# Kernel optimization log

Measured on AMD Instinct MI355X. Metric: run time of the kernel, lower is better.

Reference implementation:

```python
import jax, jax.numpy as jnp
import numpy as np
import math

EMBED = 512
NUM_CLASSES = 100000
BATCH = 512
SCALE = 64.0
MARGIN = 0.5
COS_M = math.cos(MARGIN)
SIN_M = math.sin(MARGIN)
THRESHOLD = math.cos(math.pi - MARGIN)
MARGIN_MULT = math.sin(math.pi - MARGIN) * MARGIN
EPS = 1e-12  # F.normalize eps


def setup_inputs() -> dict:
    key = jax.random.key(0)
    k1, k2, k3 = jax.random.split(key, 3)
    embeddings = jax.random.normal(k1, (BATCH, EMBED), dtype=jnp.float32)
    labels = jax.random.randint(k2, (BATCH,), 0, NUM_CLASSES, dtype=jnp.int64)
    # xavier-uniform-like init for weight (num_classes, embedding_size)
    limit = math.sqrt(6.0 / (NUM_CLASSES + EMBED))
    weight = jax.random.uniform(k3, (NUM_CLASSES, EMBED), dtype=jnp.float32,
                                minval=-limit, maxval=limit)
    return {"embeddings": embeddings, "labels": labels, "weight": weight}


def _l2_normalize(x, axis):
    norm = jnp.sqrt(jnp.sum(x * x, axis=axis, keepdims=True))
    return x / jnp.maximum(norm, EPS)


def reference(embeddings, labels, weight):
    e = _l2_normalize(embeddings, axis=1)          # (B, D)
    w = _l2_normalize(weight, axis=1)              # (C, D)
    cosine = jnp.einsum('bd,cd->bc', e, w)         # (B, C)
    sine = jnp.sqrt(jnp.clip(1.0 - cosine * cosine, 0.0, None))
    phi = cosine * COS_M - sine * SIN_M
    # easy_margin=False branch
    phi = jnp.where(cosine > THRESHOLD, phi, cosine - MARGIN_MULT)
    one_hot = jax.nn.one_hot(labels, NUM_CLASSES, dtype=cosine.dtype)
    logits = SCALE * (one_hot * phi + (1.0 - one_hot) * cosine)
    logp = jax.nn.log_softmax(logits, axis=1)      # (B, C)
    nll = -jnp.take_along_axis(logp, labels[:, None], axis=1)[:, 0]
    return jnp.mean(nll)
```

## Files before the change

kernel.cpp:

```cpp
#include <hip/hip_runtime.h>
#include <hip/hip_bf16.h>
#include <math.h>

#define BATCH 512
#define EMBED 512
#define NCLS  100000
#define NCG   128
#define NBLK  512

typedef __attribute__((ext_vector_type(4)))  float f32x4;
typedef __attribute__((ext_vector_type(16))) float f32x16;
typedef __attribute__((ext_vector_type(2)))  long  i64x2;

constexpr float kCOS_M = 0.8775825618903728f;
constexpr float kSIN_M = 0.4794255386042030f;
constexpr float kTHR   = -0.8775825618903728f;
constexpr float kMM    = 0.2397127693021015f;

#define BARRIER() asm volatile("s_waitcnt lgkmcnt(0)\n\ts_barrier" ::: "memory")

__global__ void knorm_e(const float* __restrict__ E, unsigned char* __restrict__ En8) {
  int r = blockIdx.x;
  int l = threadIdx.x;
  const f32x4* src = (const f32x4*)(E + r * EMBED);
  f32x4 a = src[2 * l], b = src[2 * l + 1];
  float ss = a.x*a.x + a.y*a.y + a.z*a.z + a.w*a.w
           + b.x*b.x + b.y*b.y + b.z*b.z + b.w*b.w;
#pragma unroll
  for (int d = 1; d < 64; d <<= 1) ss += __shfl_xor(ss, d);
  float s = 16.0f / fmaxf(sqrtf(ss), 1e-12f);
  int w0 = __builtin_amdgcn_cvt_pk_fp8_f32(a.x * s, a.y * s, 0, false);
  w0     = __builtin_amdgcn_cvt_pk_fp8_f32(a.z * s, a.w * s, w0, true);
  int w1 = __builtin_amdgcn_cvt_pk_fp8_f32(b.x * s, b.y * s, 0, false);
  w1     = __builtin_amdgcn_cvt_pk_fp8_f32(b.z * s, b.w * s, w1, true);
  int slotL = (l & 1) * 16 + (l >> 2);
  int half  = (l >> 1) & 1;
  uint2 pk; pk.x = (unsigned)w0; pk.y = (unsigned)w1;
  *(uint2*)(En8 + r * 512 + (((slotL ^ (r & 31)) << 4) | (half << 3))) = pk;
}

__global__ void klabel(const float* __restrict__ E, const float* __restrict__ W,
                       const int* __restrict__ labels,
                       float* __restrict__ lcos, float* __restrict__ lphi)
{
  int r = blockIdx.x * 8 + (threadIdx.x >> 6);
  int l = threadIdx.x & 63;
  int lbl = labels[r];
  const float* ep = E + (size_t)r * EMBED + l * 8;
  const float* wp = W + (size_t)lbl * EMBED + l * 8;
  f32x4 e0 = *(const f32x4*)ep, e1 = *(const f32x4*)(ep + 4);
  f32x4 w0 = *(const f32x4*)wp, w1 = *(const f32x4*)(wp + 4);
  float dot = e0.x*w0.x + e0.y*w0.y + e0.z*w0.z + e0.w*w0.w
            + e1.x*w1.x + e1.y*w1.y + e1.z*w1.z + e1.w*w1.w;
  float se = e0.x*e0.x + e0.y*e0.y + e0.z*e0.z + e0.w*e0.w
           + e1.x*e1.x + e1.y*e1.y + e1.z*e1.z + e1.w*e1.w;
  float sw = w0.x*w0.x + w0.y*w0.y + w0.z*w0.z + w0.w*w0.w
           + w1.x*w1.x + w1.y*w1.y + w1.z*w1.z + w1.w*w1.w;
#pragma unroll
  for (int d = 1; d < 64; d <<= 1) {
    dot += __shfl_xor(dot, d); se += __shfl_xor(se, d); sw += __shfl_xor(sw, d);
  }
  float cosv = dot / (fmaxf(sqrtf(se), 1e-12f) * fmaxf(sqrtf(sw), 1e-12f));
  float cc = fminf(fmaxf(cosv, -1.f), 1.f);
  float sine = sqrtf(fmaxf(1.f - cc * cc, 0.f));
  float phi = (cosv > kTHR) ? (cosv * kCOS_M - sine * kSIN_M) : (cosv - kMM);
  if (l == 0) { lcos[r] = 64.f * cosv; lphi[r] = 64.f * phi; }
}

__global__ __launch_bounds__(512, 4) void kmain(
    const unsigned char* __restrict__ En8, const float* __restrict__ W,
    float* __restrict__ psum)
{
  __shared__ unsigned char Asm[128 * 512];
  __shared__ unsigned char Bsm[2][4096];
  __shared__ float rowsum[64];
  __shared__ float smemS[2][128];

  int bid = blockIdx.x;
  int xcd = bid & 7;
  int panel = (bid >> 3) & 3;
  int grp = bid >> 5;
  int cg = xcd | (grp << 3);

  int tid = threadIdx.x;
  int w = tid >> 6, l = tid & 63;
  int wr = w >> 1, wc = w & 1;
  int cl = l & 31, hi = l >> 5;
  int bcls = tid >> 3, bseg = tid & 7;

  int nt = (cg < 27) ? 13 : 12;
  int nph = nt * 8;

#pragma unroll
  for (int i = 0; i < 8; ++i) {
    int base = i * 8192 + w * 1024;
    __builtin_amdgcn_global_load_lds(
        (const __attribute__((address_space(1))) void*)(En8 + panel * 65536 + base + l * 16),
        (__attribute__((address_space(3))) void*)(&Asm[base]), 16, 0, 0);
  }

  f32x4 Ra0, Ra1, Rb0, Rb1;
  float ssq = 0.f;
  const int bregion = (bseg & 1) * 2 + (bseg >> 2);
  const int bhalf = (bseg >> 1) & 1;

  auto loadB = [&](int q, f32x4& v0, f32x4& v1) {
    int T = q >> 3;
    int cls = (cg + (T << 7)) * 64 + bcls;
    if (cls >= NCLS) cls = NCLS - 1;
    const float* p = W + (size_t)cls * EMBED + (q & 7) * 64 + bseg * 8;
    v0 = *(const f32x4*)p;
    v1 = *(const f32x4*)(p + 4);
  };

  auto writeB = [&](int buf, f32x4 v0, f32x4 v1) {
    float x0 = v0.x*128.f, x1 = v0.y*128.f, x2 = v0.z*128.f, x3 = v0.w*128.f;
    float x4 = v1.x*128.f, x5 = v1.y*128.f, x6 = v1.z*128.f, x7 = v1.w*128.f;
    ssq += x0*x0 + x1*x1 + x2*x2 + x3*x3 + x4*x4 + x5*x5 + x6*x6 + x7*x7;
    int w0 = __builtin_amdgcn_cvt_pk_fp8_f32(x0, x1, 0, false);
    w0     = __builtin_amdgcn_cvt_pk_fp8_f32(x2, x3, w0, true);
    int w1 = __builtin_amdgcn_cvt_pk_fp8_f32(x4, x5, 0, false);
    w1     = __builtin_amdgcn_cvt_pk_fp8_f32(x6, x7, w1, true);
    uint2 pk; pk.x = (unsigned)w0; pk.y = (unsigned)w1;
    *(uint2*)(&Bsm[buf][bregion * 1024 + bcls * 16 + bhalf * 8]) = pk;
  };

  f32x16 acc, S;
#pragma unroll
  for (int e = 0; e < 16; ++e) { acc[e] = 0.f; S[e] = 0.f; }

  const unsigned char* Abase = &Asm[(wr * 32 + cl) * 512];
  const int arowx = cl;
  const unsigned char* Bcol0 = &Bsm[0][(hi * 2) * 1024 + (wc * 32 + cl) * 16];
  const unsigned char* Bcol1 = &Bsm[1][(hi * 2) * 1024 + (wc * 32 + cl) * 16];

  auto compute = [&](const unsigned char* bb, int pt) {
    int t0 = pt * 2;
    i64x2 a0 = *(const i64x2*)(Abase + ((((hi << 4) | t0)       ^ arowx) << 4));
    i64x2 a1 = *(const i64x2*)(Abase + ((((hi << 4) | (t0 + 1)) ^ arowx) << 4));
    i64x2 b0 = *(const i64x2*)(bb);
    i64x2 b1 = *(const i64x2*)(bb + 1024);
    acc = __builtin_amdgcn_mfma_f32_32x32x16_fp8_fp8(a0[0], b0[0], acc, 0, 0, 0);
    acc = __builtin_amdgcn_mfma_f32_32x32x16_fp8_fp8(a0[1], b0[1], acc, 0, 0, 0);
    acc = __builtin_amdgcn_mfma_f32_32x32x16_fp8_fp8(a1[0], b1[0], acc, 0, 0, 0);
    acc = __builtin_amdgcn_mfma_f32_32x32x16_fp8_fp8(a1[1], b1[1], acc, 0, 0, 0);
  };

  auto ssqred = [&]() {
    float sq = ssq;
    sq += __shfl_xor(sq, 1); sq += __shfl_xor(sq, 2); sq += __shfl_xor(sq, 4);
    if (bseg == 0) rowsum[bcls] = sq;
    ssq = 0.f;
  };

  auto epilogue = [&](int T) {
    float rs = fmaxf(rowsum[wc * 32 + cl], 1e-30f);
    float rn = 4.0f / sqrtf(rs);
    int colg = (cg + (T << 7)) * 64 + wc * 32 + cl;
    float vm = (colg < NCLS) ? 1.0f : 0.0f;
#pragma unroll
    for (int e = 0; e < 16; ++e) {
      float v = __expf(fmaf(acc[e], rn, -64.0f));
      S[e] = fmaf(v, vm, S[e]);
      acc[e] = 0.f;
    }
  };

  loadB(0, Ra0, Ra1); loadB(1, Rb0, Rb1);
  writeB(0, Ra0, Ra1); writeB(1, Rb0, Rb1);
  loadB(2, Ra0, Ra1); loadB(3, Rb0, Rb1);
  asm volatile("s_waitcnt vmcnt(0)" ::: "memory");
  BARRIER();

  for (int p = 0; p < nph; p += 2) {
    compute(Bcol0, p & 7);
    BARRIER();
    if (p + 2 < nph) writeB(0, Ra0, Ra1);
    if (p + 4 < nph) loadB(p + 4, Ra0, Ra1);
    int po = p + 1;
    compute(Bcol1, po & 7);
    if ((po & 7) == 7) epilogue(po >> 3);
    BARRIER();
    if (po + 2 < nph) writeB(1, Rb0, Rb1);
    if (po + 4 < nph) loadB(po + 4, Rb0, Rb1);
    if (((po + 2) & 7) == 7) ssqred();
  }

#pragma unroll
  for (int e = 0; e < 16; ++e) {
    float v = S[e];
    v += __shfl_xor(v, 1); v += __shfl_xor(v, 2); v += __shfl_xor(v, 4);
    v += __shfl_xor(v, 8); v += __shfl_xor(v, 16);
    S[e] = v;
  }
  __syncthreads();
  if (cl == 0) {
#pragma unroll
    for (int e = 0; e < 16; ++e) {
      int row = wr * 32 + (e & 3) + 8 * (e >> 2) + 4 * hi;
      smemS[wc][row] = S[e];
    }
  }
  __syncthreads();
  if (tid < 128) psum[bid * 128 + tid] = smemS[0][tid] + smemS[1][tid];
}

__global__ void kred1(const float* __restrict__ psum, float* __restrict__ pp2) {
  int g = blockIdx.x;
  int r = threadIdx.x;
  int panel = g >> 4, grp = g & 15;
  float s = 0.f;
#pragma unroll
  for (int x = 0; x < 8; ++x) {
    int bid = x | (panel << 3) | (grp << 5);
    s += psum[bid * 128 + r];
  }
  pp2[g * 128 + r] = s;
}

__global__ void kfinal(const float* __restrict__ pp2, const float* __restrict__ lcos,
                       const float* __restrict__ lphi, float* __restrict__ out)
{
  int tid = threadIdx.x;
  int panel = tid >> 7, rl = tid & 127;
  float S = 0.f;
#pragma unroll
  for (int grp = 0; grp < 16; ++grp)
    S += pp2[((panel << 4) | grp) * 128 + rl];
  float lc = lcos[tid], lp = lphi[tid];
  S = S - __expf(lc - 64.f) + __expf(lp - 64.f);
  float nll = 64.f + __logf(S) - lp;
#pragma unroll
  for (int d = 1; d < 64; d <<= 1) nll += __shfl_xor(nll, d);
  __shared__ float sm[8];
  if ((tid & 63) == 0) sm[tid >> 6] = nll;
  __syncthreads();
  if (tid == 0) {
    float t = 0.f;
    for (int k = 0; k < 8; ++k) t += sm[k];
    out[0] = t * (1.0f / 512.0f);
  }
}

extern "C" void kernel_launch(void* const* d_in, const int* in_sizes, int n_in,
                              void* d_out, int out_size, void* d_ws, size_t ws_size,
                              hipStream_t stream)
{
  const float* E      = (const float*)d_in[0];
  const int*   labels = (const int*)d_in[1];
  const float* W      = (const float*)d_in[2];
  float* out = (float*)d_out;

  char* ws = (char*)d_ws;
  unsigned char* En8 = (unsigned char*)ws;
  float* psum = (float*)(ws + 262144);
  float* pp2  = (float*)(ws + 524288);
  float* lcos = (float*)(ws + 557056);
  float* lphi = lcos + BATCH;

  knorm_e<<<BATCH, 64, 0, stream>>>(E, En8);
  klabel <<<64, 512, 0, stream>>>(E, W, labels, lcos, lphi);
  kmain  <<<NBLK, 512, 0, stream>>>(En8, W, psum);
  kred1  <<<64, 128, 0, stream>>>(psum, pp2);
  kfinal <<<1, 512, 0, stream>>>(pp2, lcos, lphi, out);
}
```

Before: 89.12 us.

## Feed W fragments directly from registers into MFMA, drop B LDS staging and barriers

```diff
diff --git a/kernel.cpp b/kernel.cpp
--- a/kernel.cpp
+++ b/kernel.cpp
@@ -5,8 +5,6 @@
 #define BATCH 512
 #define EMBED 512
 #define NCLS  100000
-#define NCG   128
-#define NBLK  512
 
 typedef __attribute__((ext_vector_type(4)))  float f32x4;
 typedef __attribute__((ext_vector_type(16))) float f32x16;
@@ -17,7 +15,11 @@
 constexpr float kTHR   = -0.8775825618903728f;
 constexpr float kMM    = 0.2397127693021015f;
 
-#define BARRIER() asm volatile("s_waitcnt lgkmcnt(0)\n\ts_barrier" ::: "memory")
+__device__ __forceinline__ unsigned cvt4(float a, float b, float c, float d) {
+  int v = __builtin_amdgcn_cvt_pk_fp8_f32(a, b, 0, false);
+  v = __builtin_amdgcn_cvt_pk_fp8_f32(c, d, v, true);
+  return (unsigned)v;
+}
 
 __global__ void knorm_e(const float* __restrict__ E, unsigned char* __restrict__ En8) {
   int r = blockIdx.x;
@@ -29,13 +31,11 @@
 #pragma unroll
   for (int d = 1; d < 64; d <<= 1) ss += __shfl_xor(ss, d);
   float s = 16.0f / fmaxf(sqrtf(ss), 1e-12f);
-  int w0 = __builtin_amdgcn_cvt_pk_fp8_f32(a.x * s, a.y * s, 0, false);
-  w0     = __builtin_amdgcn_cvt_pk_fp8_f32(a.z * s, a.w * s, w0, true);
-  int w1 = __builtin_amdgcn_cvt_pk_fp8_f32(b.x * s, b.y * s, 0, false);
-  w1     = __builtin_amdgcn_cvt_pk_fp8_f32(b.z * s, b.w * s, w1, true);
+  uint2 pk;
+  pk.x = cvt4(a.x * s, a.y * s, a.z * s, a.w * s);
+  pk.y = cvt4(b.x * s, b.y * s, b.z * s, b.w * s);
   int slotL = (l & 1) * 16 + (l >> 2);
   int half  = (l >> 1) & 1;
-  uint2 pk; pk.x = (unsigned)w0; pk.y = (unsigned)w1;
   *(uint2*)(En8 + r * 512 + (((slotL ^ (r & 31)) << 4) | (half << 3))) = pk;
 }
 
@@ -67,29 +67,21 @@
   if (l == 0) { lcos[r] = 64.f * cosv; lphi[r] = 64.f * phi; }
 }
 
-__global__ __launch_bounds__(512, 4) void kmain(
+__global__ __launch_bounds__(512, 1) void kmain(
     const unsigned char* __restrict__ En8, const float* __restrict__ W,
     float* __restrict__ psum)
 {
   __shared__ unsigned char Asm[128 * 512];
-  __shared__ unsigned char Bsm[2][4096];
-  __shared__ float rowsum[64];
-  __shared__ float smemS[2][128];
+  __shared__ float smemS[8][128];
 
   int bid = blockIdx.x;
-  int xcd = bid & 7;
+  int xcd  = bid & 7;
   int panel = (bid >> 3) & 3;
-  int grp = bid >> 5;
-  int cg = xcd | (grp << 3);
+  int slot = bid >> 5;
 
   int tid = threadIdx.x;
   int w = tid >> 6, l = tid & 63;
-  int wr = w >> 1, wc = w & 1;
   int cl = l & 31, hi = l >> 5;
-  int bcls = tid >> 3, bseg = tid & 7;
-
-  int nt = (cg < 27) ? 13 : 12;
-  int nph = nt * 8;
 
 #pragma unroll
   for (int i = 0; i < 8; ++i) {
@@ -99,122 +91,137 @@
         (__attribute__((address_space(3))) void*)(&Asm[base]), 16, 0, 0);
   }
 
-  f32x4 Ra0, Ra1, Rb0, Rb1;
+  const unsigned char* Ap0 = (const unsigned char*)Asm + (size_t)cl * 512;
+  const unsigned char* Ap1 = Ap0 + 32 * 512;
+  const unsigned char* Ap2 = Ap0 + 64 * 512;
+  const unsigned char* Ap3 = Ap0 + 96 * 512;
+
+  int cnt = ((3124 - xcd) >> 3) + 1;
+  int sloc0 = slot * 8 + w;
+  int njobs = (cnt - sloc0 + 63) >> 6;
+  int strip0 = xcd + 8 * sloc0;
+  const size_t JSTR = (size_t)512 * 32 * EMBED;
+  const float* wjob = W + (size_t)(strip0 * 32 + cl) * EMBED + hi * 8;
+
+  f32x4 Ra0, Ra1, Ra2, Ra3, Rb0, Rb1, Rb2, Rb3;
+  f32x4 Rc0, Rc1, Rc2, Rc3, Rd0, Rd1, Rd2, Rd3;
+  f32x16 acc0, acc1, acc2, acc3, S0, S1, S2, S3;
+#pragma unroll
+  for (int e = 0; e < 16; ++e) {
+    acc0[e] = 0.f; acc1[e] = 0.f; acc2[e] = 0.f; acc3[e] = 0.f;
+    S0[e] = 0.f; S1[e] = 0.f; S2[e] = 0.f; S3[e] = 0.f;
+  }
   float ssq = 0.f;
-  const int bregion = (bseg & 1) * 2 + (bseg >> 2);
-  const int bhalf = (bseg >> 1) & 1;
-
-  auto loadB = [&](int q, f32x4& v0, f32x4& v1) {
-    int T = q >> 3;
-    int cls = (cg + (T << 7)) * 64 + bcls;
-    if (cls >= NCLS) cls = NCLS - 1;
-    const float* p = W + (size_t)cls * EMBED + (q & 7) * 64 + bseg * 8;
-    v0 = *(const f32x4*)p;
-    v1 = *(const f32x4*)(p + 4);
-  };
-
-  auto writeB = [&](int buf, f32x4 v0, f32x4 v1) {
-    float x0 = v0.x*128.f, x1 = v0.y*128.f, x2 = v0.z*128.f, x3 = v0.w*128.f;
-    float x4 = v1.x*128.f, x5 = v1.y*128.f, x6 = v1.z*128.f, x7 = v1.w*128.f;
-    ssq += x0*x0 + x1*x1 + x2*x2 + x3*x3 + x4*x4 + x5*x5 + x6*x6 + x7*x7;
-    int w0 = __builtin_amdgcn_cvt_pk_fp8_f32(x0, x1, 0, false);
-    w0     = __builtin_amdgcn_cvt_pk_fp8_f32(x2, x3, w0, true);
-    int w1 = __builtin_amdgcn_cvt_pk_fp8_f32(x4, x5, 0, false);
-    w1     = __builtin_amdgcn_cvt_pk_fp8_f32(x6, x7, w1, true);
-    uint2 pk; pk.x = (unsigned)w0; pk.y = (unsigned)w1;
-    *(uint2*)(&Bsm[buf][bregion * 1024 + bcls * 16 + bhalf * 8]) = pk;
-  };
-
-  f32x16 acc, S;
-#pragma unroll
-  for (int e = 0; e < 16; ++e) { acc[e] = 0.f; S[e] = 0.f; }
-
-  const unsigned char* Abase = &Asm[(wr * 32 + cl) * 512];
-  const int arowx = cl;
-  const unsigned char* Bcol0 = &Bsm[0][(hi * 2) * 1024 + (wc * 32 + cl) * 16];
-  const unsigned char* Bcol1 = &Bsm[1][(hi * 2) * 1024 + (wc * 32 + cl) * 16];
-
-  auto compute = [&](const unsigned char* bb, int pt) {
-    int t0 = pt * 2;
-    i64x2 a0 = *(const i64x2*)(Abase + ((((hi << 4) | t0)       ^ arowx) << 4));
-    i64x2 a1 = *(const i64x2*)(Abase + ((((hi << 4) | (t0 + 1)) ^ arowx) << 4));
-    i64x2 b0 = *(const i64x2*)(bb);
-    i64x2 b1 = *(const i64x2*)(bb + 1024);
-    acc = __builtin_amdgcn_mfma_f32_32x32x16_fp8_fp8(a0[0], b0[0], acc, 0, 0, 0);
-    acc = __builtin_amdgcn_mfma_f32_32x32x16_fp8_fp8(a0[1], b0[1], acc, 0, 0, 0);
-    acc = __builtin_amdgcn_mfma_f32_32x32x16_fp8_fp8(a1[0], b1[0], acc, 0, 0, 0);
-    acc = __builtin_amdgcn_mfma_f32_32x32x16_fp8_fp8(a1[1], b1[1], acc, 0, 0, 0);
-  };
-
-  auto ssqred = [&]() {
-    float sq = ssq;
-    sq += __shfl_xor(sq, 1); sq += __shfl_xor(sq, 2); sq += __shfl_xor(sq, 4);
-    if (bseg == 0) rowsum[bcls] = sq;
+
+#define LOADP(R0, R1, R2, R3, base, p)                    \
+  R0 = *(const f32x4*)((base) + (p) * 32);                \
+  R1 = *(const f32x4*)((base) + (p) * 32 + 4);            \
+  R2 = *(const f32x4*)((base) + (p) * 32 + 16);           \
+  R3 = *(const f32x4*)((base) + (p) * 32 + 20);
+
+#define COMPUTEP(R0, R1, R2, R3, p) {                                          \
+    ssq += R0.x*R0.x + R0.y*R0.y + R0.z*R0.z + R0.w*R0.w                       \
+         + R1.x*R1.x + R1.y*R1.y + R1.z*R1.z + R1.w*R1.w                       \
+         + R2.x*R2.x + R2.y*R2.y + R2.z*R2.z + R2.w*R2.w                       \
+         + R3.x*R3.x + R3.y*R3.y + R3.z*R3.z + R3.w*R3.w;                      \
+    uint2 bu0, bu1;                                                            \
+    bu0.x = cvt4(R0.x*128.f, R0.y*128.f, R0.z*128.f, R0.w*128.f);              \
+    bu0.y = cvt4(R1.x*128.f, R1.y*128.f, R1.z*128.f, R1.w*128.f);              \
+    bu1.x = cvt4(R2.x*128.f, R2.y*128.f, R2.z*128.f, R2.w*128.f);              \
+    bu1.y = cvt4(R3.x*128.f, R3.y*128.f, R3.z*128.f, R3.w*128.f);              \
+    long bop0 = __builtin_bit_cast(long, bu0);                                 \
+    long bop1 = __builtin_bit_cast(long, bu1);                                 \
+    const int so = ((((hi) << 4) | (p)) ^ cl) << 4;                            \
+    i64x2 a0 = *(const i64x2*)(Ap0 + so);                                      \
+    i64x2 a1 = *(const i64x2*)(Ap1 + so);                                      \
+    i64x2 a2 = *(const i64x2*)(Ap2 + so);                                      \
+    i64x2 a3 = *(const i64x2*)(Ap3 + so);                                      \
+    acc0 = __builtin_amdgcn_mfma_f32_32x32x16_fp8_fp8(a0[0], bop0, acc0,0,0,0);\
+    acc0 = __builtin_amdgcn_mfma_f32_32x32x16_fp8_fp8(a0[1], bop1, acc0,0,0,0);\
+    acc1 = __builtin_amdgcn_mfma_f32_32x32x16_fp8_fp8(a1[0], bop0, acc1,0,0,0);\
+    acc1 = __builtin_amdgcn_mfma_f32_32x32x16_fp8_fp8(a1[1], bop1, acc1,0,0,0);\
+    acc2 = __builtin_amdgcn_mfma_f32_32x32x16_fp8_fp8(a2[0], bop0, acc2,0,0,0);\
+    acc2 = __builtin_amdgcn_mfma_f32_32x32x16_fp8_fp8(a2[1], bop1, acc2,0,0,0);\
+    acc3 = __builtin_amdgcn_mfma_f32_32x32x16_fp8_fp8(a3[0], bop0, acc3,0,0,0);\
+    acc3 = __builtin_amdgcn_mfma_f32_32x32x16_fp8_fp8(a3[1], bop1, acc3,0,0,0);\
+  }
+
+  LOADP(Ra0, Ra1, Ra2, Ra3, wjob, 0)
+  LOADP(Rb0, Rb1, Rb2, Rb3, wjob, 1)
+  LOADP(Rc0, Rc1, Rc2, Rc3, wjob, 2)
+  LOADP(Rd0, Rd1, Rd2, Rd3, wjob, 3)
+  __syncthreads();
+
+  for (int j = 0; j < njobs; ++j) {
+    const float* wnx = (j + 1 < njobs) ? (wjob + JSTR) : W;
+    COMPUTEP(Ra0, Ra1, Ra2, Ra3, 0)  LOADP(Ra0, Ra1, Ra2, Ra3, wjob, 4)
+    COMPUTEP(Rb0, Rb1, Rb2, Rb3, 1)  LOADP(Rb0, Rb1, Rb2, Rb3, wjob, 5)
+    COMPUTEP(Rc0, Rc1, Rc2, Rc3, 2)  LOADP(Rc0, Rc1, Rc2, Rc3, wjob, 6)
+    COMPUTEP(Rd0, Rd1, Rd2, Rd3, 3)  LOADP(Rd0, Rd1, Rd2, Rd3, wjob, 7)
+    COMPUTEP(Ra0, Ra1, Ra2, Ra3, 4)  LOADP(Ra0, Ra1, Ra2, Ra3, wjob, 8)
+    COMPUTEP(Rb0, Rb1, Rb2, Rb3, 5)  LOADP(Rb0, Rb1, Rb2, Rb3, wjob, 9)
+    COMPUTEP(Rc0, Rc1, Rc2, Rc3, 6)  LOADP(Rc0, Rc1, Rc2, Rc3, wjob, 10)
+    COMPUTEP(Rd0, Rd1, Rd2, Rd3, 7)  LOADP(Rd0, Rd1, Rd2, Rd3, wjob, 11)
+    COMPUTEP(Ra0, Ra1, Ra2, Ra3, 8)  LOADP(Ra0, Ra1, Ra2, Ra3, wjob, 12)
+    COMPUTEP(Rb0, Rb1, Rb2, Rb3, 9)  LOADP(Rb0, Rb1, Rb2, Rb3, wjob, 13)
+    COMPUTEP(Rc0, Rc1, Rc2, Rc3, 10) LOADP(Rc0, Rc1, Rc2, Rc3, wjob, 14)
+    COMPUTEP(Rd0, Rd1, Rd2, Rd3, 11) LOADP(Rd0, Rd1, Rd2, Rd3, wjob, 15)
+    COMPUTEP(Ra0, Ra1, Ra2, Ra3, 12) LOADP(Ra0, Ra1, Ra2, Ra3, wnx, 0)
+    COMPUTEP(Rb0, Rb1, Rb2, Rb3, 13) LOADP(Rb0, Rb1, Rb2, Rb3, wnx, 1)
+    COMPUTEP(Rc0, Rc1, Rc2, Rc3, 14) LOADP(Rc0, Rc1, Rc2, Rc3, wnx, 2)
+    COMPUTEP(Rd0, Rd1, Rd2, Rd3, 15) LOADP(Rd0, Rd1, Rd2, Rd3, wnx, 3)
+    float rs = ssq + __shfl_xor(ssq, 32);
+    float rn = 0.03125f * rsqrtf(fmaxf(rs, 1e-30f));
+#pragma unroll
+    for (int e = 0; e < 16; ++e) {
+      S0[e] += __expf(fmaf(acc0[e], rn, -64.f)); acc0[e] = 0.f;
+      S1[e] += __expf(fmaf(acc1[e], rn, -64.f)); acc1[e] = 0.f;
+      S2[e] += __expf(fmaf(acc2[e], rn, -64.f)); acc2[e] = 0.f;
+      S3[e] += __expf(fmaf(acc3[e], rn, -64.f)); acc3[e] = 0.f;
+    }
     ssq = 0.f;
-  };
-
-  auto epilogue = [&](int T) {
-    float rs = fmaxf(rowsum[wc * 32 + cl], 1e-30f);
-    float rn = 4.0f / sqrtf(rs);
-    int colg = (cg + (T << 7)) * 64 + wc * 32 + cl;
-    float vm = (colg < NCLS) ? 1.0f : 0.0f;
+    wjob = wnx;
+  }
+#undef LOADP
+#undef COMPUTEP
+
+#pragma unroll
+  for (int e = 0; e < 16; ++e) {
+    float v0 = S0[e], v1 = S1[e], v2 = S2[e], v3 = S3[e];
+#pragma unroll
+    for (int d = 1; d < 32; d <<= 1) {
+      v0 += __shfl_xor(v0, d); v1 += __shfl_xor(v1, d);
+      v2 += __shfl_xor(v2, d); v3 += __shfl_xor(v3, d);
+    }
+    S0[e] = v0; S1[e] = v1; S2[e] = v2; S3[e] = v3;
+  }
+  if (cl == 0) {
 #pragma unroll
     for (int e = 0; e < 16; ++e) {
-      float v = __expf(fmaf(acc[e], rn, -64.0f));
-      S[e] = fmaf(v, vm, S[e]);
-      acc[e] = 0.f;
+      int rmap = (e & 3) + 8 * (e >> 2) + 4 * hi;
+      smemS[w][rmap]      = S0[e];
+      smemS[w][32 + rmap] = S1[e];
+      smemS[w][64 + rmap] = S2[e];
+      smemS[w][96 + rmap] = S3[e];
     }
-  };
-
-  loadB(0, Ra0, Ra1); loadB(1, Rb0, Rb1);
-  writeB(0, Ra0, Ra1); writeB(1, Rb0, Rb1);
-  loadB(2, Ra0, Ra1); loadB(3, Rb0, Rb1);
-  asm volatile("s_waitcnt vmcnt(0)" ::: "memory");
-  BARRIER();
-
-  for (int p = 0; p < nph; p += 2) {
-    compute(Bcol0, p & 7);
-    BARRIER();
-    if (p + 2 < nph) writeB(0, Ra0, Ra1);
-    if (p + 4 < nph) loadB(p + 4, Ra0, Ra1);
-    int po = p + 1;
-    compute(Bcol1, po & 7);
-    if ((po & 7) == 7) epilogue(po >> 3);
-    BARRIER();
-    if (po + 2 < nph) writeB(1, Rb0, Rb1);
-    if (po + 4 < nph) loadB(po + 4, Rb0, Rb1);
-    if (((po + 2) & 7) == 7) ssqred();
-  }
-
-#pragma unroll
-  for (int e = 0; e < 16; ++e) {
-    float v = S[e];
-    v += __shfl_xor(v, 1); v += __shfl_xor(v, 2); v += __shfl_xor(v, 4);
-    v += __shfl_xor(v, 8); v += __shfl_xor(v, 16);
-    S[e] = v;
   }
   __syncthreads();
-  if (cl == 0) {
-#pragma unroll
-    for (int e = 0; e < 16; ++e) {
-      int row = wr * 32 + (e & 3) + 8 * (e >> 2) + 4 * hi;
-      smemS[wc][row] = S[e];
-    }
-  }
-  __syncthreads();
-  if (tid < 128) psum[bid * 128 + tid] = smemS[0][tid] + smemS[1][tid];
+  if (tid < 128) {
+    float t = 0.f;
+#pragma unroll
+    for (int q = 0; q < 8; ++q) t += smemS[q][tid];
+    psum[bid * 128 + tid] = t;
+  }
 }
 
 __global__ void kred1(const float* __restrict__ psum, float* __restrict__ pp2) {
   int g = blockIdx.x;
   int r = threadIdx.x;
-  int panel = g >> 4, grp = g & 15;
+  int panel = g >> 3, xcd = g & 7;
   float s = 0.f;
 #pragma unroll
-  for (int x = 0; x < 8; ++x) {
-    int bid = x | (panel << 3) | (grp << 5);
-    s += psum[bid * 128 + r];
-  }
+  for (int slot = 0; slot < 8; ++slot)
+    s += psum[(xcd + 8 * panel + 32 * slot) * 128 + r];
   pp2[g * 128 + r] = s;
 }
 
@@ -225,8 +232,8 @@
   int panel = tid >> 7, rl = tid & 127;
   float S = 0.f;
 #pragma unroll
-  for (int grp = 0; grp < 16; ++grp)
-    S += pp2[((panel << 4) | grp) * 128 + rl];
+  for (int x = 0; x < 8; ++x)
+    S += pp2[(panel * 8 + x) * 128 + rl];
   float lc = lcos[tid], lp = lphi[tid];
   S = S - __expf(lc - 64.f) + __expf(lp - 64.f);
   float nll = 64.f + __logf(S) - lp;
@@ -254,13 +261,13 @@
   char* ws = (char*)d_ws;
   unsigned char* En8 = (unsigned char*)ws;
   float* psum = (float*)(ws + 262144);
-  float* pp2  = (float*)(ws + 524288);
-  float* lcos = (float*)(ws + 557056);
+  float* pp2  = (float*)(ws + 262144 + 131072);
+  float* lcos = (float*)(ws + 262144 + 131072 + 16384);
   float* lphi = lcos + BATCH;
 
   knorm_e<<<BATCH, 64, 0, stream>>>(E, En8);
   klabel <<<64, 512, 0, stream>>>(E, W, labels, lcos, lphi);
-  kmain  <<<NBLK, 512, 0, stream>>>(En8, W, psum);
-  kred1  <<<64, 128, 0, stream>>>(psum, pp2);
+  kmain  <<<256, 512, 0, stream>>>(En8, W, psum);
+  kred1  <<<32, 128, 0, stream>>>(psum, pp2);
   kfinal <<<1, 512, 0, stream>>>(pp2, lcos, lphi, out);
 }
```

Result: slower. 279.1 us (+213.2%).

## Hold normalized embedding panel in registers instead of LDS, unroll phase loop

Applied to the files above, without the earlier changes.

```diff
diff --git a/kernel.cpp b/kernel.cpp
--- a/kernel.cpp
+++ b/kernel.cpp
@@ -18,6 +18,12 @@
 constexpr float kMM    = 0.2397127693021015f;
 
 #define BARRIER() asm volatile("s_waitcnt lgkmcnt(0)\n\ts_barrier" ::: "memory")
+
+__device__ __forceinline__ unsigned cvt4(float a, float b, float c, float d) {
+  int v = __builtin_amdgcn_cvt_pk_fp8_f32(a, b, 0, false);
+  v = __builtin_amdgcn_cvt_pk_fp8_f32(c, d, v, true);
+  return (unsigned)v;
+}
 
 __global__ void knorm_e(const float* __restrict__ E, unsigned char* __restrict__ En8) {
   int r = blockIdx.x;
@@ -29,14 +35,12 @@
 #pragma unroll
   for (int d = 1; d < 64; d <<= 1) ss += __shfl_xor(ss, d);
   float s = 16.0f / fmaxf(sqrtf(ss), 1e-12f);
-  int w0 = __builtin_amdgcn_cvt_pk_fp8_f32(a.x * s, a.y * s, 0, false);
-  w0     = __builtin_amdgcn_cvt_pk_fp8_f32(a.z * s, a.w * s, w0, true);
-  int w1 = __builtin_amdgcn_cvt_pk_fp8_f32(b.x * s, b.y * s, 0, false);
-  w1     = __builtin_amdgcn_cvt_pk_fp8_f32(b.z * s, b.w * s, w1, true);
+  uint2 pk;
+  pk.x = cvt4(a.x * s, a.y * s, a.z * s, a.w * s);
+  pk.y = cvt4(b.x * s, b.y * s, b.z * s, b.w * s);
   int slotL = (l & 1) * 16 + (l >> 2);
   int half  = (l >> 1) & 1;
-  uint2 pk; pk.x = (unsigned)w0; pk.y = (unsigned)w1;
-  *(uint2*)(En8 + r * 512 + (((slotL ^ (r & 31)) << 4) | (half << 3))) = pk;
+  *(uint2*)(En8 + r * 512 + ((slotL << 4) | (half << 3))) = pk;
 }
 
 __global__ void klabel(const float* __restrict__ E, const float* __restrict__ W,
@@ -71,7 +75,6 @@
     const unsigned char* __restrict__ En8, const float* __restrict__ W,
     float* __restrict__ psum)
 {
-  __shared__ unsigned char Asm[128 * 512];
   __shared__ unsigned char Bsm[2][4096];
   __shared__ float rowsum[64];
   __shared__ float smemS[2][128];
@@ -89,102 +92,91 @@
   int bcls = tid >> 3, bseg = tid & 7;
 
   int nt = (cg < 27) ? 13 : 12;
-  int nph = nt * 8;
-
-#pragma unroll
-  for (int i = 0; i < 8; ++i) {
-    int base = i * 8192 + w * 1024;
-    __builtin_amdgcn_global_load_lds(
-        (const __attribute__((address_space(1))) void*)(En8 + panel * 65536 + base + l * 16),
-        (__attribute__((address_space(3))) void*)(&Asm[base]), 16, 0, 0);
-  }
+
+  int arow = panel * 128 + wr * 32 + cl;
+  const unsigned char* abase = En8 + arow * 512 + hi * 256;
+  i64x2 af[16];
+#pragma unroll
+  for (int t = 0; t < 16; ++t) af[t] = *(const i64x2*)(abase + t * 16);
+
+  float ssq = 0.f;
+  const int boff = ((bseg & 1) * 2 + (bseg >> 2)) * 1024 + bcls * 16 + ((bseg >> 1) & 1) * 8;
 
   f32x4 Ra0, Ra1, Rb0, Rb1;
-  float ssq = 0.f;
-  const int bregion = (bseg & 1) * 2 + (bseg >> 2);
-  const int bhalf = (bseg >> 1) & 1;
-
-  auto loadB = [&](int q, f32x4& v0, f32x4& v1) {
-    int T = q >> 3;
+  auto loadB = [&](int T, int kt, f32x4& v0, f32x4& v1) {
     int cls = (cg + (T << 7)) * 64 + bcls;
     if (cls >= NCLS) cls = NCLS - 1;
-    const float* p = W + (size_t)cls * EMBED + (q & 7) * 64 + bseg * 8;
+    const float* p = W + (size_t)cls * EMBED + kt * 64 + bseg * 8;
     v0 = *(const f32x4*)p;
     v1 = *(const f32x4*)(p + 4);
   };
-
   auto writeB = [&](int buf, f32x4 v0, f32x4 v1) {
     float x0 = v0.x*128.f, x1 = v0.y*128.f, x2 = v0.z*128.f, x3 = v0.w*128.f;
     float x4 = v1.x*128.f, x5 = v1.y*128.f, x6 = v1.z*128.f, x7 = v1.w*128.f;
     ssq += x0*x0 + x1*x1 + x2*x2 + x3*x3 + x4*x4 + x5*x5 + x6*x6 + x7*x7;
-    int w0 = __builtin_amdgcn_cvt_pk_fp8_f32(x0, x1, 0, false);
-    w0     = __builtin_amdgcn_cvt_pk_fp8_f32(x2, x3, w0, true);
-    int w1 = __builtin_amdgcn_cvt_pk_fp8_f32(x4, x5, 0, false);
-    w1     = __builtin_amdgcn_cvt_pk_fp8_f32(x6, x7, w1, true);
-    uint2 pk; pk.x = (unsigned)w0; pk.y = (unsigned)w1;
-    *(uint2*)(&Bsm[buf][bregion * 1024 + bcls * 16 + bhalf * 8]) = pk;
+    uint2 pk;
+    pk.x = cvt4(x0, x1, x2, x3);
+    pk.y = cvt4(x4, x5, x6, x7);
+    *(uint2*)(&Bsm[buf][boff]) = pk;
   };
 
   f32x16 acc, S;
 #pragma unroll
   for (int e = 0; e < 16; ++e) { acc[e] = 0.f; S[e] = 0.f; }
 
-  const unsigned char* Abase = &Asm[(wr * 32 + cl) * 512];
-  const int arowx = cl;
   const unsigned char* Bcol0 = &Bsm[0][(hi * 2) * 1024 + (wc * 32 + cl) * 16];
   const unsigned char* Bcol1 = &Bsm[1][(hi * 2) * 1024 + (wc * 32 + cl) * 16];
 
-  auto compute = [&](const unsigned char* bb, int pt) {
-    int t0 = pt * 2;
-    i64x2 a0 = *(const i64x2*)(Abase + ((((hi << 4) | t0)       ^ arowx) << 4));
-    i64x2 a1 = *(const i64x2*)(Abase + ((((hi << 4) | (t0 + 1)) ^ arowx) << 4));
-    i64x2 b0 = *(const i64x2*)(bb);
-    i64x2 b1 = *(const i64x2*)(bb + 1024);
-    acc = __builtin_amdgcn_mfma_f32_32x32x16_fp8_fp8(a0[0], b0[0], acc, 0, 0, 0);
-    acc = __builtin_amdgcn_mfma_f32_32x32x16_fp8_fp8(a0[1], b0[1], acc, 0, 0, 0);
-    acc = __builtin_amdgcn_mfma_f32_32x32x16_fp8_fp8(a1[0], b1[0], acc, 0, 0, 0);
-    acc = __builtin_amdgcn_mfma_f32_32x32x16_fp8_fp8(a1[1], b1[1], acc, 0, 0, 0);
-  };
-
-  auto ssqred = [&]() {
-    float sq = ssq;
-    sq += __shfl_xor(sq, 1); sq += __shfl_xor(sq, 2); sq += __shfl_xor(sq, 4);
-    if (bseg == 0) rowsum[bcls] = sq;
-    ssq = 0.f;
-  };
-
-  auto epilogue = [&](int T) {
-    float rs = fmaxf(rowsum[wc * 32 + cl], 1e-30f);
-    float rn = 4.0f / sqrtf(rs);
-    int colg = (cg + (T << 7)) * 64 + wc * 32 + cl;
-    float vm = (colg < NCLS) ? 1.0f : 0.0f;
-#pragma unroll
-    for (int e = 0; e < 16; ++e) {
-      float v = __expf(fmaf(acc[e], rn, -64.0f));
-      S[e] = fmaf(v, vm, S[e]);
-      acc[e] = 0.f;
-    }
-  };
-
-  loadB(0, Ra0, Ra1); loadB(1, Rb0, Rb1);
-  writeB(0, Ra0, Ra1); writeB(1, Rb0, Rb1);
-  loadB(2, Ra0, Ra1); loadB(3, Rb0, Rb1);
-  asm volatile("s_waitcnt vmcnt(0)" ::: "memory");
-  BARRIER();
-
-  for (int p = 0; p < nph; p += 2) {
-    compute(Bcol0, p & 7);
-    BARRIER();
-    if (p + 2 < nph) writeB(0, Ra0, Ra1);
-    if (p + 4 < nph) loadB(p + 4, Ra0, Ra1);
-    int po = p + 1;
-    compute(Bcol1, po & 7);
-    if ((po & 7) == 7) epilogue(po >> 3);
-    BARRIER();
-    if (po + 2 < nph) writeB(1, Rb0, Rb1);
-    if (po + 4 < nph) loadB(po + 4, Rb0, Rb1);
-    if (((po + 2) & 7) == 7) ssqred();
-  }
+  loadB(0, 0, Ra0, Ra1);
+  loadB(0, 1, Rb0, Rb1);
+  writeB(0, Ra0, Ra1);
+  writeB(1, Rb0, Rb1);
+  loadB(0, 2, Ra0, Ra1);
+  loadB(0, 3, Rb0, Rb1);
+  __syncthreads();
+
+#define PHASE(q, RS0, RS1) {                                                          \
+    const unsigned char* bb = ((q) & 1) ? Bcol1 : Bcol0;                              \
+    i64x2 b0 = *(const i64x2*)(bb);                                                   \
+    i64x2 b1 = *(const i64x2*)(bb + 1024);                                            \
+    acc = __builtin_amdgcn_mfma_f32_32x32x16_fp8_fp8(af[2*(q)][0],   b0[0], acc,0,0,0);\
+    acc = __builtin_amdgcn_mfma_f32_32x32x16_fp8_fp8(af[2*(q)][1],   b0[1], acc,0,0,0);\
+    acc = __builtin_amdgcn_mfma_f32_32x32x16_fp8_fp8(af[2*(q)+1][0], b1[0], acc,0,0,0);\
+    acc = __builtin_amdgcn_mfma_f32_32x32x16_fp8_fp8(af[2*(q)+1][1], b1[1], acc,0,0,0);\
+    if ((q) == 7) {                                                                    \
+      float rs = fmaxf(rowsum[wc * 32 + cl], 1e-30f);                                  \
+      float rn = 4.0f / sqrtf(rs);                                                     \
+      int colg = (cg + (T << 7)) * 64 + wc * 32 + cl;                                  \
+      float vm = (colg < NCLS) ? 1.0f : 0.0f;                                          \
+      _Pragma("unroll")                                                                \
+      for (int e = 0; e < 16; ++e) {                                                   \
+        S[e] = fmaf(__expf(fmaf(acc[e], rn, -64.0f)), vm, S[e]);                       \
+        acc[e] = 0.f;                                                                  \
+      }                                                                                \
+    }                                                                                  \
+    BARRIER();                                                                         \
+    if (!lastT || (q) < 6) writeB((q) & 1, RS0, RS1);                                  \
+    if (!lastT || (q) < 4) loadB(T + (((q) + 4) >> 3), ((q) + 4) & 7, RS0, RS1);       \
+    if ((q) == 5) {                                                                    \
+      float sq = ssq;                                                                  \
+      sq += __shfl_xor(sq, 1); sq += __shfl_xor(sq, 2); sq += __shfl_xor(sq, 4);       \
+      if (bseg == 0) rowsum[bcls] = sq;                                                \
+      ssq = 0.f;                                                                       \
+    }                                                                                  \
+  }
+
+  for (int T = 0; T < nt; ++T) {
+    bool lastT = (T == nt - 1);
+    PHASE(0, Ra0, Ra1)
+    PHASE(1, Rb0, Rb1)
+    PHASE(2, Ra0, Ra1)
+    PHASE(3, Rb0, Rb1)
+    PHASE(4, Ra0, Ra1)
+    PHASE(5, Rb0, Rb1)
+    PHASE(6, Ra0, Ra1)
+    PHASE(7, Rb0, Rb1)
+  }
+#undef PHASE
 
 #pragma unroll
   for (int e = 0; e < 16; ++e) {
```

Result: slower. 107.6 us (+20.7%).

## Enlarge main kernel tile to 256 rows with 1024-thread blocks

Applied to the files above, without the earlier changes.

```diff
diff --git a/kernel.cpp b/kernel.cpp
--- a/kernel.cpp
+++ b/kernel.cpp
@@ -6,7 +6,7 @@
 #define EMBED 512
 #define NCLS  100000
 #define NCG   128
-#define NBLK  512
+#define NBLK  256
 
 typedef __attribute__((ext_vector_type(4)))  float f32x4;
 typedef __attribute__((ext_vector_type(16))) float f32x16;
@@ -18,6 +18,12 @@
 constexpr float kMM    = 0.2397127693021015f;
 
 #define BARRIER() asm volatile("s_waitcnt lgkmcnt(0)\n\ts_barrier" ::: "memory")
+
+__device__ __forceinline__ unsigned cvt4(float a, float b, float c, float d) {
+  int v = __builtin_amdgcn_cvt_pk_fp8_f32(a, b, 0, false);
+  v = __builtin_amdgcn_cvt_pk_fp8_f32(c, d, v, true);
+  return (unsigned)v;
+}
 
 __global__ void knorm_e(const float* __restrict__ E, unsigned char* __restrict__ En8) {
   int r = blockIdx.x;
@@ -29,13 +35,11 @@
 #pragma unroll
   for (int d = 1; d < 64; d <<= 1) ss += __shfl_xor(ss, d);
   float s = 16.0f / fmaxf(sqrtf(ss), 1e-12f);
-  int w0 = __builtin_amdgcn_cvt_pk_fp8_f32(a.x * s, a.y * s, 0, false);
-  w0     = __builtin_amdgcn_cvt_pk_fp8_f32(a.z * s, a.w * s, w0, true);
-  int w1 = __builtin_amdgcn_cvt_pk_fp8_f32(b.x * s, b.y * s, 0, false);
-  w1     = __builtin_amdgcn_cvt_pk_fp8_f32(b.z * s, b.w * s, w1, true);
+  uint2 pk;
+  pk.x = cvt4(a.x * s, a.y * s, a.z * s, a.w * s);
+  pk.y = cvt4(b.x * s, b.y * s, b.z * s, b.w * s);
   int slotL = (l & 1) * 16 + (l >> 2);
   int half  = (l >> 1) & 1;
-  uint2 pk; pk.x = (unsigned)w0; pk.y = (unsigned)w1;
   *(uint2*)(En8 + r * 512 + (((slotL ^ (r & 31)) << 4) | (half << 3))) = pk;
 }
 
@@ -67,62 +71,52 @@
   if (l == 0) { lcos[r] = 64.f * cosv; lphi[r] = 64.f * phi; }
 }
 
-__global__ __launch_bounds__(512, 4) void kmain(
+__global__ __launch_bounds__(1024, 4) void kmain(
     const unsigned char* __restrict__ En8, const float* __restrict__ W,
     float* __restrict__ psum)
 {
-  __shared__ unsigned char Asm[128 * 512];
-  __shared__ unsigned char Bsm[2][4096];
+  __shared__ __align__(16) unsigned char Asm[256 * 512];
+  __shared__ __align__(16) unsigned char Bsm[2][4096];
   __shared__ float rowsum[64];
-  __shared__ float smemS[2][128];
+  __shared__ float smemS[2][256];
 
   int bid = blockIdx.x;
   int xcd = bid & 7;
-  int panel = (bid >> 3) & 3;
-  int grp = bid >> 5;
+  int panel = (bid >> 3) & 1;
+  int grp = bid >> 4;
   int cg = xcd | (grp << 3);
 
   int tid = threadIdx.x;
   int w = tid >> 6, l = tid & 63;
   int wr = w >> 1, wc = w & 1;
   int cl = l & 31, hi = l >> 5;
-  int bcls = tid >> 3, bseg = tid & 7;
+  int bcls = tid >> 4, bs = tid & 15;
 
   int nt = (cg < 27) ? 13 : 12;
   int nph = nt * 8;
 
 #pragma unroll
   for (int i = 0; i < 8; ++i) {
-    int base = i * 8192 + w * 1024;
+    int base = i * 16384 + w * 1024;
     __builtin_amdgcn_global_load_lds(
-        (const __attribute__((address_space(1))) void*)(En8 + panel * 65536 + base + l * 16),
+        (const __attribute__((address_space(1))) void*)(En8 + panel * 131072 + base + l * 16),
         (__attribute__((address_space(3))) void*)(&Asm[base]), 16, 0, 0);
   }
 
-  f32x4 Ra0, Ra1, Rb0, Rb1;
   float ssq = 0.f;
-  const int bregion = (bseg & 1) * 2 + (bseg >> 2);
-  const int bhalf = (bseg >> 1) & 1;
-
-  auto loadB = [&](int q, f32x4& v0, f32x4& v1) {
-    int T = q >> 3;
-    int cls = (cg + (T << 7)) * 64 + bcls;
+  const int boff = (((bs >> 1) & 1) * 2 + (bs >> 3)) * 1024 + bcls * 16
+                 + ((bs >> 2) & 1) * 8 + (bs & 1) * 4;
+
+  f32x4 Ra, Rb;
+  auto loadB = [&](int q, f32x4& v) {
+    int cls = (cg + ((q >> 3) << 7)) * 64 + bcls;
     if (cls >= NCLS) cls = NCLS - 1;
-    const float* p = W + (size_t)cls * EMBED + (q & 7) * 64 + bseg * 8;
-    v0 = *(const f32x4*)p;
-    v1 = *(const f32x4*)(p + 4);
-  };
-
-  auto writeB = [&](int buf, f32x4 v0, f32x4 v1) {
-    float x0 = v0.x*128.f, x1 = v0.y*128.f, x2 = v0.z*128.f, x3 = v0.w*128.f;
-    float x4 = v1.x*128.f, x5 = v1.y*128.f, x6 = v1.z*128.f, x7 = v1.w*128.f;
-    ssq += x0*x0 + x1*x1 + x2*x2 + x3*x3 + x4*x4 + x5*x5 + x6*x6 + x7*x7;
-    int w0 = __builtin_amdgcn_cvt_pk_fp8_f32(x0, x1, 0, false);
-    w0     = __builtin_amdgcn_cvt_pk_fp8_f32(x2, x3, w0, true);
-    int w1 = __builtin_amdgcn_cvt_pk_fp8_f32(x4, x5, 0, false);
-    w1     = __builtin_amdgcn_cvt_pk_fp8_f32(x6, x7, w1, true);
-    uint2 pk; pk.x = (unsigned)w0; pk.y = (unsigned)w1;
-    *(uint2*)(&Bsm[buf][bregion * 1024 + bcls * 16 + bhalf * 8]) = pk;
+    v = *(const f32x4*)(W + (size_t)cls * EMBED + (q & 7) * 64 + bs * 4);
+  };
+  auto writeB = [&](int buf, f32x4 v) {
+    float x0 = v.x*128.f, x1 = v.y*128.f, x2 = v.z*128.f, x3 = v.w*128.f;
+    ssq += x0*x0 + x1*x1 + x2*x2 + x3*x3;
+    *(unsigned*)(&Bsm[buf][boff]) = cvt4(x0, x1, x2, x3);
   };
 
   f32x16 acc, S;
@@ -130,14 +124,13 @@
   for (int e = 0; e < 16; ++e) { acc[e] = 0.f; S[e] = 0.f; }
 
   const unsigned char* Abase = &Asm[(wr * 32 + cl) * 512];
-  const int arowx = cl;
   const unsigned char* Bcol0 = &Bsm[0][(hi * 2) * 1024 + (wc * 32 + cl) * 16];
   const unsigned char* Bcol1 = &Bsm[1][(hi * 2) * 1024 + (wc * 32 + cl) * 16];
 
   auto compute = [&](const unsigned char* bb, int pt) {
     int t0 = pt * 2;
-    i64x2 a0 = *(const i64x2*)(Abase + ((((hi << 4) | t0)       ^ arowx) << 4));
-    i64x2 a1 = *(const i64x2*)(Abase + ((((hi << 4) | (t0 + 1)) ^ arowx) << 4));
+    i64x2 a0 = *(const i64x2*)(Abase + ((((hi << 4) | t0)       ^ cl) << 4));
+    i64x2 a1 = *(const i64x2*)(Abase + ((((hi << 4) | (t0 + 1)) ^ cl) << 4));
     i64x2 b0 = *(const i64x2*)(bb);
     i64x2 b1 = *(const i64x2*)(bb + 1024);
     acc = __builtin_amdgcn_mfma_f32_32x32x16_fp8_fp8(a0[0], b0[0], acc, 0, 0, 0);
@@ -148,8 +141,9 @@
 
   auto ssqred = [&]() {
     float sq = ssq;
-    sq += __shfl_xor(sq, 1); sq += __shfl_xor(sq, 2); sq += __shfl_xor(sq, 4);
-    if (bseg == 0) rowsum[bcls] = sq;
+    sq += __shfl_xor(sq, 1); sq += __shfl_xor(sq, 2);
+    sq += __shfl_xor(sq, 4); sq += __shfl_xor(sq, 8);
+    if (bs == 0) rowsum[bcls] = sq;
     ssq = 0.f;
   };
 
@@ -160,29 +154,28 @@
     float vm = (colg < NCLS) ? 1.0f : 0.0f;
 #pragma unroll
     for (int e = 0; e < 16; ++e) {
-      float v = __expf(fmaf(acc[e], rn, -64.0f));
-      S[e] = fmaf(v, vm, S[e]);
+      S[e] = fmaf(__expf(fmaf(acc[e], rn, -64.0f)), vm, S[e]);
       acc[e] = 0.f;
     }
   };
 
-  loadB(0, Ra0, Ra1); loadB(1, Rb0, Rb1);
-  writeB(0, Ra0, Ra1); writeB(1, Rb0, Rb1);
-  loadB(2, Ra0, Ra1); loadB(3, Rb0, Rb1);
+  loadB(0, Ra); loadB(1, Rb);
+  writeB(0, Ra); writeB(1, Rb);
+  loadB(2, Ra); loadB(3, Rb);
   asm volatile("s_waitcnt vmcnt(0)" ::: "memory");
   BARRIER();
 
   for (int p = 0; p < nph; p += 2) {
     compute(Bcol0, p & 7);
     BARRIER();
-    if (p + 2 < nph) writeB(0, Ra0, Ra1);
-    if (p + 4 < nph) loadB(p + 4, Ra0, Ra1);
+    if (p + 2 < nph) writeB(0, Ra);
+    if (p + 4 < nph) loadB(p + 4, Ra);
     int po = p + 1;
     compute(Bcol1, po & 7);
     if ((po & 7) == 7) epilogue(po >> 3);
     BARRIER();
-    if (po + 2 < nph) writeB(1, Rb0, Rb1);
-    if (po + 4 < nph) loadB(po + 4, Rb0, Rb1);
+    if (po + 2 < nph) writeB(1, Rb);
+    if (po + 4 < nph) loadB(po + 4, Rb);
     if (((po + 2) & 7) == 7) ssqred();
   }
 
@@ -202,7 +195,7 @@
     }
   }
   __syncthreads();
-  if (tid < 128) psum[bid * 128 + tid] = smemS[0][tid] + smemS[1][tid];
+  if (tid < 256) psum[bid * 256 + tid] = smemS[0][tid] + smemS[1][tid];
 }
 
 __global__ void kred1(const float* __restrict__ psum, float* __restrict__ pp2) {
@@ -212,21 +205,21 @@
   float s = 0.f;
 #pragma unroll
   for (int x = 0; x < 8; ++x) {
-    int bid = x | (panel << 3) | (grp << 5);
-    s += psum[bid * 128 + r];
-  }
-  pp2[g * 128 + r] = s;
+    int bid = x | (panel << 3) | (grp << 4);
+    s += psum[bid * 256 + r];
+  }
+  pp2[g * 256 + r] = s;
 }
 
 __global__ void kfinal(const float* __restrict__ pp2, const float* __restrict__ lcos,
                        const float* __restrict__ lphi, float* __restrict__ out)
 {
   int tid = threadIdx.x;
-  int panel = tid >> 7, rl = tid & 127;
+  int panel = tid >> 8, rl = tid & 255;
   float S = 0.f;
 #pragma unroll
   for (int grp = 0; grp < 16; ++grp)
-    S += pp2[((panel << 4) | grp) * 128 + rl];
+    S += pp2[((panel << 4) | grp) * 256 + rl];
   float lc = lcos[tid], lp = lphi[tid];
   S = S - __expf(lc - 64.f) + __expf(lp - 64.f);
   float nll = 64.f + __logf(S) - lp;
@@ -260,7 +253,7 @@
 
   knorm_e<<<BATCH, 64, 0, stream>>>(E, En8);
   klabel <<<64, 512, 0, stream>>>(E, W, labels, lcos, lphi);
-  kmain  <<<NBLK, 512, 0, stream>>>(En8, W, psum);
-  kred1  <<<64, 128, 0, stream>>>(psum, pp2);
+  kmain  <<<NBLK, 1024, 0, stream>>>(En8, W, psum);
+  kred1  <<<32, 256, 0, stream>>>(psum, pp2);
   kfinal <<<1, 512, 0, stream>>>(pp2, lcos, lphi, out);
 }
```

Result: faster. 86.63 us (-2.8%).
